# Kernel tuning notes

Hardware: AMD Instinct MI355X
Metric: run time of the kernel (lower is better)

The kernel has to match this reference:

```python
import jax, jax.numpy as jnp
import numpy as np
import math

B, S, D, H = 4, 2048, 2048, 16
HD = D // H

def setup_inputs() -> dict:
    key = jax.random.key(0)
    ks = jax.random.split(key, 8)
    scale = 1.0 / math.sqrt(D)
    return {
        "query": jax.random.normal(ks[0], (B, S, D), jnp.float32),
        "key": jax.random.normal(ks[1], (B, S, D), jnp.float32),
        "value": jax.random.normal(ks[2], (B, S, D), jnp.float32),
        "attention_mask": jnp.ones((B, S), jnp.int32),
        "Wq": jax.random.normal(ks[3], (D, D), jnp.float32) * scale,
        "Wk": jax.random.normal(ks[4], (D, D), jnp.float32) * scale,
        "Wv": jax.random.normal(ks[5], (D, D), jnp.float32) * scale,
        "Wo": jax.random.normal(ks[6], (D, D), jnp.float32) * scale,
    }

def reference(query, key, value, attention_mask, Wq, Wk, Wv, Wo):
    b, sq, d = query.shape
    sk = key.shape[1]
    # nn.Linear(bias=False): y = x @ W.T, W is [out, in]
    Q = (query @ Wq.T).reshape(b, sq, H, HD).transpose(0, 2, 1, 3)  # [b,h,sq,hd]
    K = (key @ Wk.T).reshape(b, sk, H, HD).transpose(0, 2, 1, 3)
    V = (value @ Wv.T).reshape(b, sk, H, HD).transpose(0, 2, 1, 3)
    scores = jnp.einsum('bhqd,bhkd->bhqk', Q, K) / math.sqrt(HD)
    causal = jnp.tril(jnp.ones((sq, sk), dtype=bool))  # mask_future=True
    scores = jnp.where(causal[None, None, :, :], scores, jnp.float32(-10000.0))
    pad = (attention_mask != 0)[:, None, None, :]  # [b,1,1,sk]
    scores = jnp.where(pad, scores, jnp.float32(-10000.0))
    w = jax.nn.softmax(scores, axis=-1)  # dropout is identity in eval mode
    out = jnp.einsum('bhqk,bhkd->bhqd', w, V)
    out = out.transpose(0, 2, 1, 3).reshape(b, sq, d)
    return out @ Wo.T
```

## Files before the change

kernel.cpp:

```cpp
#include <hip/hip_runtime.h>
#include <hip/hip_bf16.h>

#define NB 4
#define NS 2048
#define ND 2048
#define NH 16
#define NHD 128

#define QSCALE 0.12751746f

typedef __bf16 bf16x8 __attribute__((ext_vector_type(8)));
typedef float f32x4 __attribute__((ext_vector_type(4)));

#define MFMA16(a, b, c) __builtin_amdgcn_mfma_f32_16x16x32_bf16((a), (b), (c), 0, 0, 0)

#define GLOAD_LDS16(gptr, lptr)                                              \
  __builtin_amdgcn_global_load_lds(                                          \
      (const __attribute__((address_space(1))) unsigned int*)(gptr),         \
      (__attribute__((address_space(3))) unsigned int*)(lptr), 16, 0, 0)

static __device__ __forceinline__ ushort f2bf(float f) {
  union { float f; unsigned u; } v; v.f = f;
  unsigned r = v.u + 0x7fffu + ((v.u >> 16) & 1u);
  return (ushort)(r >> 16);
}

static __device__ __forceinline__ float exp2_fast(float x) {
  float r;
  asm("v_exp_f32 %0, %1" : "=v"(r) : "v"(x));
  return r;
}

static __device__ __forceinline__ unsigned cvtpk(float lo, float hi) {
  unsigned r;
  asm("v_cvt_pk_bf16_f32 %0, %1, %2" : "=v"(r) : "v"(lo), "v"(hi));
  return r;
}

__global__ __launch_bounds__(256) void cvt_all_kernel(
    const float* __restrict__ q, const float* __restrict__ k,
    const float* __restrict__ v, const float* __restrict__ wq,
    const float* __restrict__ wk, const float* __restrict__ wv,
    const float* __restrict__ wo, ushort* __restrict__ tokdst,
    ushort* __restrict__ wdst, ushort* __restrict__ wodst, int nw) {
  const int n8t = 1 << 21, n8w = 1 << 19;
  const int total = 3 * n8t + nw * n8w;
  int i = blockIdx.x * blockDim.x + threadIdx.x;
  const int stride = gridDim.x * blockDim.x;
  for (; i < total; i += stride) {
    const float* s;
    uint4* d;
    int e;
    if (i < 3 * n8t) {
      const int j = i >> 21;
      s = (j == 0) ? q : ((j == 1) ? k : v);
      e = i & (n8t - 1);
      d = (uint4*)tokdst + i;
    } else {
      const int i2 = i - 3 * n8t;
      const int j = i2 >> 19;
      e = i2 & (n8w - 1);
      if (j < 3) {
        s = (j == 0) ? wq : ((j == 1) ? wk : wv);
        d = (uint4*)wdst + i2;
      } else {
        s = wo;
        d = (uint4*)wodst + e;
      }
    }
    float4 a = ((const float4*)s)[e * 2];
    float4 b = ((const float4*)s)[e * 2 + 1];
    uint4 u;
    u.x = cvtpk(a.x, a.y);
    u.y = cvtpk(a.z, a.w);
    u.z = cvtpk(b.x, b.y);
    u.w = cvtpk(b.z, b.w);
    *d = u;
  }
}

__global__ __launch_bounds__(256) void cvt_kernel(const float* __restrict__ in,
                                                  ushort* __restrict__ out,
                                                  int n8) {
  int i = blockIdx.x * blockDim.x + threadIdx.x;
  const int stride = gridDim.x * blockDim.x;
  for (; i < n8; i += stride) {
    float4 a = ((const float4*)in)[i * 2];
    float4 b = ((const float4*)in)[i * 2 + 1];
    uint4 u;
    u.x = cvtpk(a.x, a.y);
    u.y = cvtpk(a.z, a.w);
    u.z = cvtpk(b.x, b.y);
    u.w = cvtpk(b.z, b.w);
    ((uint4*)out)[i] = u;
  }
}

static __device__ __forceinline__ void gemm256_loop(
    const ushort* __restrict__ A, const ushort* __restrict__ W,
    ushort* smem, int m0, int n0, f32x4 (&acc)[8][4]) {
  constexpr int K = ND;
  constexpr int NT = K / 64;
  const int tid = threadIdx.x;
  const int lane = tid & 63;
  const int w = tid >> 6;
  const int lr = lane & 15;
  const int lg = lane >> 4;
  const int wm = w >> 2;
  const int wn = w & 3;

  const int srow = tid >> 3;
  const int sg = (tid & 7) ^ (srow & 7);
  const ushort* ga = &A[(size_t)(m0 + srow) * K + sg * 8];
  const ushort* gb = &W[(size_t)(n0 + srow) * K + sg * 8];

  auto gA = [&](int kt, int r) {
    ushort* la = &smem[(kt & 1) * 16384 + tid * 8];
    GLOAD_LDS16(ga + (size_t)(r * 64) * K + kt * 64, la + r * 4096);
  };
  auto gB = [&](int kt, int r) {
    ushort* lb = &smem[32768 + (kt & 1) * 16384 + tid * 8];
    GLOAD_LDS16(gb + (size_t)(r * 64) * K + kt * 64, lb + r * 4096);
  };

  const int g0 = lg ^ (lr & 7);
  const int g1 = (4 + lg) ^ (lr & 7);

  bf16x8 Bf[4][2];
  auto readB = [&](int buf) {
    const ushort* Bb = &smem[32768 + buf * 16384];
#pragma unroll
    for (int nf = 0; nf < 4; ++nf) {
      const int brow = wn * 64 + nf * 16 + lr;
      Bf[nf][0] = *(const bf16x8*)&Bb[brow * 64 + g0 * 8];
      Bf[nf][1] = *(const bf16x8*)&Bb[brow * 64 + g1 * 8];
    }
  };
  auto readA = [&](int buf, int q, bf16x8 (&a)[2][2]) {
    const ushort* Ab = &smem[buf * 16384];
#pragma unroll
    for (int j = 0; j < 2; ++j) {
      const int arow = wm * 128 + (2 * q + j) * 16 + lr;
      a[j][0] = *(const bf16x8*)&Ab[arow * 64 + g0 * 8];
      a[j][1] = *(const bf16x8*)&Ab[arow * 64 + g1 * 8];
    }
  };
  auto mfma_q = [&](int q, bf16x8 (&a)[2][2]) {
    __builtin_amdgcn_s_setprio(1);
#pragma unroll
    for (int j = 0; j < 2; ++j)
#pragma unroll
      for (int nf = 0; nf < 4; ++nf) {
        acc[2 * q + j][nf] = MFMA16(a[j][0], Bf[nf][0], acc[2 * q + j][nf]);
        acc[2 * q + j][nf] = MFMA16(a[j][1], Bf[nf][1], acc[2 * q + j][nf]);
      }
    __builtin_amdgcn_s_setprio(0);
  };

#pragma unroll
  for (int r = 0; r < 4; ++r) { gA(0, r); gB(0, r); }
#pragma unroll
  for (int r = 0; r < 4; ++r) { gA(1, r); gB(1, r); }
  asm volatile("s_waitcnt vmcnt(8)" ::: "memory");
  __builtin_amdgcn_s_barrier();

#pragma unroll 1
  for (int t = 0; t < NT; ++t) {
    const int c = t & 1;
    const bool s2 = (t + 2 < NT);
    {
      bf16x8 a[2][2];
      readB(c);
      readA(c, 0, a);
      if (t >= 1 && t + 1 < NT) { gA(t + 1, 1); gA(t + 1, 3); }
      asm volatile("s_waitcnt lgkmcnt(8)" ::: "memory");
      __builtin_amdgcn_s_barrier();
      mfma_q(0, a);
      __builtin_amdgcn_s_barrier();
    }
    {
      bf16x8 a[2][2];
      readA(c, 1, a);
      if (s2) { gB(t + 2, 0); gB(t + 2, 1); }
      __builtin_amdgcn_s_barrier();
      mfma_q(1, a);
      __builtin_amdgcn_s_barrier();
    }
    {
      bf16x8 a[2][2];
      readA(c, 2, a);
      if (s2) { gB(t + 2, 2); gB(t + 2, 3); }
      __builtin_amdgcn_s_barrier();
      mfma_q(2, a);
      __builtin_amdgcn_s_barrier();
    }
    {
      bf16x8 a[2][2];
      readA(c, 3, a);
      if (s2) {
        gA(t + 2, 0); gA(t + 2, 2);
        asm volatile("s_waitcnt vmcnt(6)" ::: "memory");
      } else if (t + 1 < NT) {
        asm volatile("s_waitcnt vmcnt(0)" ::: "memory");
      }
      __builtin_amdgcn_s_barrier();
      mfma_q(3, a);
      __builtin_amdgcn_s_barrier();
    }
  }
}

__global__ __launch_bounds__(512) void proj_all_kernel(
    const ushort* __restrict__ Aq, const ushort* __restrict__ Ak,
    const ushort* __restrict__ Av, const ushort* __restrict__ Wq,
    const ushort* __restrict__ Wk, const ushort* __restrict__ Wv,
    ushort* __restrict__ Cq, ushort* __restrict__ Ck,
    ushort* __restrict__ Vt, int mode_base) {
  __shared__ __align__(16) ushort smem[65536];

  const int tid = threadIdx.x;
  const int lane = tid & 63;
  const int w = tid >> 6;
  const int lr = lane & 15;
  const int lg = lane >> 4;
  const int wm = w >> 2;
  const int wn = w & 3;

  const int mode = mode_base + (int)(blockIdx.x >> 8);
  const ushort* A = (mode == 0) ? Aq : ((mode == 1) ? Ak : Av);
  const ushort* W = (mode == 0) ? Wq : ((mode == 1) ? Wk : Wv);

  const int bid = blockIdx.x & 255;
  const int l = (bid & 7) * 32 + (bid >> 3);
  const int m0 = (l >> 3) * 256;
  const int n0 = (l & 7) * 256;

  f32x4 acc[8][4];
#pragma unroll
  for (int mf = 0; mf < 8; ++mf)
#pragma unroll
    for (int nf = 0; nf < 4; ++nf) acc[mf][nf] = (f32x4){0.f, 0.f, 0.f, 0.f};

  gemm256_loop(A, W, smem, m0, n0, acc);

  if (mode < 2) {
    ushort* C = (mode == 0) ? Cq : Ck;
    const float osc = (mode == 0) ? QSCALE : 1.0f;
#pragma unroll
    for (int mf = 0; mf < 8; ++mf) {
#pragma unroll
      for (int i = 0; i < 4; ++i) {
        const size_t row = (size_t)(m0 + wm * 128 + mf * 16 + lg * 4 + i);
        ushort* op = C + row * ND + n0 + wn * 64 + lr;
#pragma unroll
        for (int nf = 0; nf < 4; ++nf)
          op[nf * 16] = f2bf(acc[mf][nf][i] * osc);
      }
    }
  } else {
    const int b = m0 >> 11;
    const int s0 = m0 & (NS - 1);
#pragma unroll 1
    for (int p = 0; p < 2; ++p) {
      if ((wn >> 1) == p) {
        const int colbase = (wn & 1) * 64;
#pragma unroll
        for (int mf = 0; mf < 8; ++mf) {
          const int sbase = wm * 128 + (mf >> 2) * 64 + (mf & 3);
#pragma unroll
          for (int i = 0; i < 4; ++i) {
            const int sp = sbase + (lg * 4 + i) * 4;
#pragma unroll
            for (int nf = 0; nf < 4; ++nf)
              smem[(colbase + nf * 16 + lr) * 264 + sp] = f2bf(acc[mf][nf][i]);
          }
        }
      }
      __syncthreads();
      const int bh = b * NH + (n0 >> 7) + p;
      const int row = tid >> 2;
      const int soff = (tid & 3) * 64;
      ushort* dst = &Vt[((size_t)bh * NHD + row) * NS + s0 + soff];
      const ushort* src = &smem[row * 264 + soff];
#pragma unroll
      for (int kq = 0; kq < 8; ++kq)
        *(uint4*)&dst[kq * 8] = *(const uint4*)&src[kq * 8];
      __syncthreads();
    }
  }
}

__global__ __launch_bounds__(512) void oproj256_kernel(
    const ushort* __restrict__ A, const ushort* __restrict__ W,
    float* __restrict__ Cv) {
  __shared__ __align__(16) ushort smem[65536];

  const int tid = threadIdx.x;
  const int lane = tid & 63;
  const int w = tid >> 6;
  const int lr = lane & 15;
  const int lg = lane >> 4;
  const int wm = w >> 2;
  const int wn = w & 3;

  const int bid = blockIdx.x;
  const int l = (bid & 7) * 32 + (bid >> 3);
  const int m0 = (l >> 3) * 256;
  const int n0 = (l & 7) * 256;

  f32x4 acc[8][4];
#pragma unroll
  for (int mf = 0; mf < 8; ++mf)
#pragma unroll
    for (int nf = 0; nf < 4; ++nf) acc[mf][nf] = (f32x4){0.f, 0.f, 0.f, 0.f};

  gemm256_loop(A, W, smem, m0, n0, acc);

#pragma unroll
  for (int mf = 0; mf < 8; ++mf) {
#pragma unroll
    for (int i = 0; i < 4; ++i) {
      const size_t row = (size_t)(m0 + wm * 128 + mf * 16 + lg * 4 + i);
      float* op = Cv + row * ND + n0 + wn * 64 + lr;
#pragma unroll
      for (int nf = 0; nf < 4; ++nf) op[nf * 16] = acc[mf][nf][i];
    }
  }
}

__global__ __launch_bounds__(512) void attn_kernel(
    const ushort* __restrict__ Qb, const ushort* __restrict__ Kb,
    const ushort* __restrict__ VtG, ushort* __restrict__ Ctx) {
  __shared__ __align__(16) ushort KL[2][64 * 128];
  __shared__ __align__(16) ushort VL[2][128 * 64];
  __shared__ __align__(16) ushort Plds[8][32][72];

  const int tid = threadIdx.x;
  const int lane = tid & 63;
  const int w = tid >> 6;
  const int lr = lane & 15;
  const int lg = lane >> 4;
  const int xk = (lr & 7) << 3;

  const int lid = blockIdx.x;
  const int nid = (lid & 7) * 32 + (lid >> 3);
  const int bh = nid >> 2;
  const int pair = nid & 3;

  const int b = bh >> 4, h = bh & 15;
  const size_t base = (size_t)b * NS * ND + (size_t)h * NHD;
  const size_t vbase = (size_t)bh * NHD * NS;
  const ushort* Qp = Qb + base;
  const ushort* Kp = Kb + base;

  const int tK = tid >> 4;
  const int cKs = ((tid & 15) << 3) ^ ((tK & 7) << 3);
  const ushort* kg = Kp + (size_t)tK * ND + cKs;
  const int tV = tid >> 3;
  const int cVs = ((tid & 7) << 3) ^ ((tV & 7) << 3);
  const ushort* vg = VtG + vbase + (size_t)tV * NS + cVs;

  auto issue = [&](int c, int buf) {
    const ushort* kgc = kg + (size_t)(c << 6) * ND;
    const ushort* vgc = vg + (c << 6);
    ushort* kl = &KL[buf][tid * 8];
    ushort* vl = &VL[buf][tid * 8];
    GLOAD_LDS16(kgc, kl);
    GLOAD_LDS16(kgc + (size_t)32 * ND, kl + 4096);
    GLOAD_LDS16(vgc, vl);
    GLOAD_LDS16(vgc + (size_t)64 * NS, vl + 4096);
  };

  int cur = 0;
#pragma unroll 1
  for (int ph = 0; ph < 2; ++ph) {
    const int qt = ph == 0 ? pair : 7 - pair;
    const int q0 = qt * 256;
    const int qbase = q0 + w * 32;

    bf16x8 qf[2][4];
#pragma unroll
    for (int m = 0; m < 2; ++m)
#pragma unroll
      for (int kk = 0; kk < 4; ++kk)
        qf[m][kk] = *(const bf16x8*)&Qp[(size_t)(qbase + m * 16 + lr) * ND +
                                        kk * 32 + lg * 8];

    float srow[2][4];
    f32x4 ctx[2][8];
#pragma unroll
    for (int m = 0; m < 2; ++m)
#pragma unroll
      for (int i = 0; i < 4; ++i) srow[m][i] = 0.f;
#pragma unroll
    for (int m = 0; m < 2; ++m)
#pragma unroll
      for (int f = 0; f < 8; ++f) ctx[m][f] = (f32x4){0.f, 0.f, 0.f, 0.f};

    const int NC = (q0 + 256) >> 6;
    issue(0, cur);
    __syncthreads();

    for (int c = 0; c < NC; ++c) {
      const int kc0 = c << 6;
      if (c + 1 < NC) issue(c + 1, cur ^ 1);

      if (kc0 <= qbase + 31) {
        const ushort* Kc = &KL[cur][0];
        const ushort* Vc = &VL[cur][0];
        f32x4 sc[2][4];
#pragma unroll
        for (int m = 0; m < 2; ++m)
#pragma unroll
          for (int n = 0; n < 4; ++n) sc[m][n] = (f32x4){0.f, 0.f, 0.f, 0.f};
        __builtin_amdgcn_s_setprio(1);
#pragma unroll
        for (int kk = 0; kk < 4; ++kk)
#pragma unroll
          for (int n = 0; n < 4; ++n) {
            bf16x8 kf = *(const bf16x8*)&Kc[(n * 16 + lr) * 128 +
                                            ((kk * 32 + lg * 8) ^ xk)];
            sc[0][n] = MFMA16(qf[0][kk], kf, sc[0][n]);
            sc[1][n] = MFMA16(qf[1][kk], kf, sc[1][n]);
          }
        __builtin_amdgcn_s_setprio(0);

#pragma unroll
        for (int m = 0; m < 2; ++m) {
          if (kc0 + 63 <= qbase + m * 16) {
#pragma unroll
            for (int i = 0; i < 4; ++i) {
              const float p0 = exp2_fast(sc[m][0][i]);
              const float p1 = exp2_fast(sc[m][1][i]);
              const float p2 = exp2_fast(sc[m][2][i]);
              const float p3 = exp2_fast(sc[m][3][i]);
              srow[m][i] += (p0 + p1) + (p2 + p3);
              uint2 pk;
              pk.x = cvtpk(p0, p1);
              pk.y = cvtpk(p2, p3);
              *(uint2*)&Plds[w][m * 16 + lg * 4 + i][lr * 4] = pk;
            }
          } else {
#pragma unroll
            for (int i = 0; i < 4; ++i) {
              const int rg = qbase + m * 16 + lg * 4 + i;
              float p[4];
#pragma unroll
              for (int n = 0; n < 4; ++n) {
                float e = exp2_fast(sc[m][n][i]);
                p[n] = (kc0 + n * 16 + lr <= rg) ? e : 0.f;
              }
              srow[m][i] += (p[0] + p[1]) + (p[2] + p[3]);
              uint2 pk;
              pk.x = cvtpk(p[0], p[1]);
              pk.y = cvtpk(p[2], p[3]);
              *(uint2*)&Plds[w][m * 16 + lg * 4 + i][lr * 4] = pk;
            }
          }
        }

        __builtin_amdgcn_s_setprio(1);
#pragma unroll
        for (int ks = 0; ks < 2; ++ks) {
          bf16x8 pa0 = *(const bf16x8*)&Plds[w][lr][ks * 32 + lg * 8];
          bf16x8 pa1 = *(const bf16x8*)&Plds[w][16 + lr][ks * 32 + lg * 8];
#pragma unroll
          for (int f = 0; f < 8; ++f) {
            bf16x8 vf = *(const bf16x8*)&Vc[(f * 16 + lr) * 64 +
                                            ((ks * 32 + lg * 8) ^ xk)];
            ctx[0][f] = MFMA16(pa0, vf, ctx[0][f]);
            ctx[1][f] = MFMA16(pa1, vf, ctx[1][f]);
          }
        }
        __builtin_amdgcn_s_setprio(0);
      }
      __syncthreads();
      cur ^= 1;
    }

#pragma unroll
    for (int m = 0; m < 2; ++m)
#pragma unroll
      for (int i = 0; i < 4; ++i) {
        float rs = srow[m][i];
        rs += __shfl_xor(rs, 1);
        rs += __shfl_xor(rs, 2);
        rs += __shfl_xor(rs, 4);
        rs += __shfl_xor(rs, 8);
        const float inv = 1.0f / rs;
        const int rg = qbase + m * 16 + lg * 4 + i;
        ushort* op = Ctx + base + (size_t)rg * ND;
#pragma unroll
        for (int f = 0; f < 8; ++f) op[f * 16 + lr] = f2bf(ctx[m][f][i] * inv);
      }
  }
}

extern "C" void kernel_launch(void* const* d_in, const int* in_sizes, int n_in,
                              void* d_out, int out_size, void* d_ws,
                              size_t ws_size, hipStream_t stream) {
  const float* q = (const float*)d_in[0];
  const float* k = (const float*)d_in[1];
  const float* v = (const float*)d_in[2];
  const float* wq = (const float*)d_in[4];
  const float* wk = (const float*)d_in[5];
  const float* wv = (const float*)d_in[6];
  const float* wo = (const float*)d_in[7];
  float* out = (float*)d_out;

  const size_t tok = (size_t)NB * NS * ND;
  const size_t wsz = (size_t)ND * ND;
  ushort* X0 = (ushort*)d_ws;
  ushort* X1 = X0 + tok;
  ushort* X2 = X1 + tok;
  ushort* X3 = X2 + tok;
  ushort* X4 = X3 + tok;
  ushort* WOb = X4 + tok;
  ushort* WQ = (ushort*)d_out;
  ushort* WK = WQ + wsz;
  ushort* WV = WK + wsz;
  ushort* Y = WV + wsz;

  const bool bigws = ws_size >= (5 * tok + wsz) * sizeof(ushort);
  dim3 cg(2048);

  if (bigws) {
    cvt_all_kernel<<<cg, 256, 0, stream>>>(q, k, v, wq, wk, wv, wo, X0, WQ,
                                           WOb, 4);
    proj_all_kernel<<<dim3(768), 512, 0, stream>>>(X0, X1, X2, WQ, WK, WV, X3,
                                                   Y, X4, 0);
    attn_kernel<<<dim3(256), 512, 0, stream>>>(X3, Y, X4, X2);
    oproj256_kernel<<<dim3(256), 512, 0, stream>>>(X2, WOb, out);
  } else {
    cvt_all_kernel<<<cg, 256, 0, stream>>>(q, k, v, wq, wk, wv, wo, X0, WQ,
                                           WOb, 3);
    proj_all_kernel<<<dim3(512), 512, 0, stream>>>(X0, X1, X2, WQ, WK, WV, X3,
                                                   Y, X1, 0);
    proj_all_kernel<<<dim3(256), 512, 0, stream>>>(X0, X1, X2, WQ, WK, WV, X3,
                                                   Y, X1, 2);
    attn_kernel<<<dim3(256), 512, 0, stream>>>(X3, Y, X1, X2);
    cvt_kernel<<<cg, 256, 0, stream>>>(wo, X0, (int)(wsz / 8));
    oproj256_kernel<<<dim3(256), 512, 0, stream>>>(X2, X0, out);
  }
}
```

Before: 433.0 us.

## Halve GEMM K-tile to 32 to shrink LDS footprint for two-block occupancy

```diff
diff --git a/kernel.cpp b/kernel.cpp
--- a/kernel.cpp
+++ b/kernel.cpp
@@ -100,7 +100,7 @@
     const ushort* __restrict__ A, const ushort* __restrict__ W,
     ushort* smem, int m0, int n0, f32x4 (&acc)[8][4]) {
   constexpr int K = ND;
-  constexpr int NT = K / 64;
+  constexpr int NT = K / 32;
   const int tid = threadIdx.x;
   const int lane = tid & 63;
   const int w = tid >> 6;
@@ -109,102 +109,79 @@
   const int wm = w >> 2;
   const int wn = w & 3;
 
-  const int srow = tid >> 3;
-  const int sg = (tid & 7) ^ (srow & 7);
-  const ushort* ga = &A[(size_t)(m0 + srow) * K + sg * 8];
-  const ushort* gb = &W[(size_t)(n0 + srow) * K + sg * 8];
-
-  auto gA = [&](int kt, int r) {
-    ushort* la = &smem[(kt & 1) * 16384 + tid * 8];
-    GLOAD_LDS16(ga + (size_t)(r * 64) * K + kt * 64, la + r * 4096);
-  };
-  auto gB = [&](int kt, int r) {
-    ushort* lb = &smem[32768 + (kt & 1) * 16384 + tid * 8];
-    GLOAD_LDS16(gb + (size_t)(r * 64) * K + kt * 64, lb + r * 4096);
-  };
-
-  const int g0 = lg ^ (lr & 7);
-  const int g1 = (4 + lg) ^ (lr & 7);
-
-  bf16x8 Bf[4][2];
+  const int tq = tid >> 2;
+  const int r0 = tq + (tq & 64);
+  const int sg = (tid & 3) ^ ((r0 >> 1) & 3);
+  const ushort* ga = &A[(size_t)(m0 + r0) * K + sg * 8];
+  const ushort* gb = &W[(size_t)(n0 + r0) * K + sg * 8];
+
+  auto gAL = [&](int kt, int L) {
+    ushort* la = &smem[(kt & 1) * 8192 + L * 4096 + tid * 8];
+    GLOAD_LDS16(ga + (size_t)(L * 64) * K + kt * 32, la);
+  };
+  auto gBL = [&](int kt, int L) {
+    ushort* lb = &smem[16384 + (kt & 1) * 8192 + L * 4096 + tid * 8];
+    GLOAD_LDS16(gb + (size_t)(L * 64) * K + kt * 32, lb);
+  };
+
+  const int lxor = (lr >> 1) & 3;
+  auto aoff = [&](int R0) {
+    const int L = (R0 >> 6) & 1;
+    const int t2b = (R0 & 63) + ((R0 >> 7) << 6);
+    return L * 4096 + (t2b + lr) * 32 + ((lg ^ lxor) << 3);
+  };
+
+  bf16x8 Bf[4];
   auto readB = [&](int buf) {
-    const ushort* Bb = &smem[32768 + buf * 16384];
-#pragma unroll
-    for (int nf = 0; nf < 4; ++nf) {
-      const int brow = wn * 64 + nf * 16 + lr;
-      Bf[nf][0] = *(const bf16x8*)&Bb[brow * 64 + g0 * 8];
-      Bf[nf][1] = *(const bf16x8*)&Bb[brow * 64 + g1 * 8];
-    }
-  };
-  auto readA = [&](int buf, int q, bf16x8 (&a)[2][2]) {
-    const ushort* Ab = &smem[buf * 16384];
-#pragma unroll
-    for (int j = 0; j < 2; ++j) {
-      const int arow = wm * 128 + (2 * q + j) * 16 + lr;
-      a[j][0] = *(const bf16x8*)&Ab[arow * 64 + g0 * 8];
-      a[j][1] = *(const bf16x8*)&Ab[arow * 64 + g1 * 8];
-    }
-  };
-  auto mfma_q = [&](int q, bf16x8 (&a)[2][2]) {
+    const ushort* Bb = &smem[16384 + buf * 8192];
+#pragma unroll
+    for (int nf = 0; nf < 4; ++nf)
+      Bf[nf] = *(const bf16x8*)&Bb[aoff(wn * 64 + nf * 16)];
+  };
+  auto readA4 = [&](int buf, int h, bf16x8 (&a)[4]) {
+    const ushort* Ab = &smem[buf * 8192];
+#pragma unroll
+    for (int j = 0; j < 4; ++j)
+      a[j] = *(const bf16x8*)&Ab[aoff(wm * 128 + (h * 4 + j) * 16)];
+  };
+  auto mfma_h = [&](int h, bf16x8 (&a)[4]) {
     __builtin_amdgcn_s_setprio(1);
 #pragma unroll
-    for (int j = 0; j < 2; ++j)
-#pragma unroll
-      for (int nf = 0; nf < 4; ++nf) {
-        acc[2 * q + j][nf] = MFMA16(a[j][0], Bf[nf][0], acc[2 * q + j][nf]);
-        acc[2 * q + j][nf] = MFMA16(a[j][1], Bf[nf][1], acc[2 * q + j][nf]);
-      }
+    for (int j = 0; j < 4; ++j)
+#pragma unroll
+      for (int nf = 0; nf < 4; ++nf)
+        acc[h * 4 + j][nf] = MFMA16(a[j], Bf[nf], acc[h * 4 + j][nf]);
     __builtin_amdgcn_s_setprio(0);
   };
 
-#pragma unroll
-  for (int r = 0; r < 4; ++r) { gA(0, r); gB(0, r); }
-#pragma unroll
-  for (int r = 0; r < 4; ++r) { gA(1, r); gB(1, r); }
-  asm volatile("s_waitcnt vmcnt(8)" ::: "memory");
+  gAL(0, 0); gAL(0, 1); gBL(0, 0); gBL(0, 1);
+  gAL(1, 0); gBL(1, 0); gBL(1, 1);
+  asm volatile("s_waitcnt vmcnt(3)" ::: "memory");
   __builtin_amdgcn_s_barrier();
 
 #pragma unroll 1
   for (int t = 0; t < NT; ++t) {
     const int c = t & 1;
-    const bool s2 = (t + 2 < NT);
     {
-      bf16x8 a[2][2];
+      bf16x8 a[4];
       readB(c);
-      readA(c, 0, a);
-      if (t >= 1 && t + 1 < NT) { gA(t + 1, 1); gA(t + 1, 3); }
-      asm volatile("s_waitcnt lgkmcnt(8)" ::: "memory");
+      readA4(c, 0, a);
+      if (t + 1 < NT) gAL(t + 1, 1);
       __builtin_amdgcn_s_barrier();
-      mfma_q(0, a);
+      mfma_h(0, a);
       __builtin_amdgcn_s_barrier();
     }
     {
-      bf16x8 a[2][2];
-      readA(c, 1, a);
-      if (s2) { gB(t + 2, 0); gB(t + 2, 1); }
-      __builtin_amdgcn_s_barrier();
-      mfma_q(1, a);
-      __builtin_amdgcn_s_barrier();
-    }
-    {
-      bf16x8 a[2][2];
-      readA(c, 2, a);
-      if (s2) { gB(t + 2, 2); gB(t + 2, 3); }
-      __builtin_amdgcn_s_barrier();
-      mfma_q(2, a);
-      __builtin_amdgcn_s_barrier();
-    }
-    {
-      bf16x8 a[2][2];
-      readA(c, 3, a);
-      if (s2) {
-        gA(t + 2, 0); gA(t + 2, 2);
-        asm volatile("s_waitcnt vmcnt(6)" ::: "memory");
+      bf16x8 a[4];
+      readA4(c, 1, a);
+      if (t + 2 < NT) {
+        gAL(t + 2, 0); gBL(t + 2, 0); gBL(t + 2, 1);
+        asm volatile("s_waitcnt vmcnt(3)" ::: "memory");
       } else if (t + 1 < NT) {
         asm volatile("s_waitcnt vmcnt(0)" ::: "memory");
       }
       __builtin_amdgcn_s_barrier();
-      mfma_q(3, a);
+      mfma_h(1, a);
       __builtin_amdgcn_s_barrier();
     }
   }
@@ -216,7 +193,7 @@
     const ushort* __restrict__ Wk, const ushort* __restrict__ Wv,
     ushort* __restrict__ Cq, ushort* __restrict__ Ck,
     ushort* __restrict__ Vt, int mode_base) {
-  __shared__ __align__(16) ushort smem[65536];
+  __shared__ __align__(16) ushort smem[33792];
 
   const int tid = threadIdx.x;
   const int lane = tid & 63;
@@ -260,6 +237,7 @@
   } else {
     const int b = m0 >> 11;
     const int s0 = m0 & (NS - 1);
+    __syncthreads();
 #pragma unroll 1
     for (int p = 0; p < 2; ++p) {
       if ((wn >> 1) == p) {
@@ -293,7 +271,7 @@
 __global__ __launch_bounds__(512) void oproj256_kernel(
     const ushort* __restrict__ A, const ushort* __restrict__ W,
     float* __restrict__ Cv) {
-  __shared__ __align__(16) ushort smem[65536];
+  __shared__ __align__(16) ushort smem[32768];
 
   const int tid = threadIdx.x;
   const int lane = tid & 63;
```

New measurement: 470.5 us. 1.09x slower.
